# Performance work log

Measured on AMD Instinct MI355X. Metric: run time of the kernel, lower is better.

Reference implementation:

```python
import jax, jax.numpy as jnp
import numpy as np

IN_F = 4096
OUT_F = 4096
NNZ = int(0.01 * IN_F * OUT_F)
ALPHA = 1.0


def setup_inputs() -> dict:
    key = jax.random.key(0)
    k1, k2, k3, k4, k5 = jax.random.split(key, 5)
    x = jax.random.normal(k1, (4, 2048, IN_F), dtype=jnp.float32)
    base_weights = (jax.random.normal(k2, (OUT_F, IN_F), dtype=jnp.float32) * 0.02).astype(jnp.float16)
    # sparse outlier correction in COO form (equivalent content to the CSR buffers)
    ortho_vals = (jax.random.normal(k3, (NNZ,), dtype=jnp.float32) * 1e-3).astype(jnp.float16)
    ortho_rows = jax.random.randint(k4, (NNZ,), 0, OUT_F, dtype=jnp.int32)
    ortho_cols = jax.random.randint(k5, (NNZ,), 0, IN_F, dtype=jnp.int32)
    return {"x": x, "base_weights": base_weights, "ortho_vals": ortho_vals,
            "ortho_rows": ortho_rows, "ortho_cols": ortho_cols}


def reference(x, base_weights, ortho_vals, ortho_rows, ortho_cols):
    orig_shape = x.shape
    orig_dtype = x.dtype
    x_flat = x.reshape(-1, IN_F)  # [N, in]

    # Base stream: fp16 GEMM, then cast to fp32 (matches torch.mm on fp16)
    out_base = jnp.matmul(x_flat.astype(jnp.float16), base_weights.T).astype(jnp.float32)

    # Ortho stream: sparse (out,in) correction applied in fp32.
    # Scatter the sparse values into a dense fp32 matrix once (cheap: 64MB),
    # then use a dense GEMM — same math as torch.sparse.mm(W_csr, x^T)^T.
    w_ortho = jnp.zeros((OUT_F, IN_F), dtype=jnp.float32).at[ortho_rows, ortho_cols].add(
        ortho_vals.astype(jnp.float32))
    out_ortho = jnp.matmul(x_flat.astype(jnp.float32), w_ortho.T)  # [N, out]

    out_flat = out_base + ALPHA * out_ortho
    return out_flat.reshape(orig_shape[:-1] + (OUT_F,)).astype(orig_dtype)
```

## Files before the change

kernel.cpp:

```cpp
#include <hip/hip_runtime.h>

typedef _Float16 f16;
typedef unsigned short u16;
typedef unsigned int u32;
typedef long long i64;
typedef __attribute__((ext_vector_type(8))) _Float16 f16x8;
typedef __attribute__((ext_vector_type(4))) float f32x4;
typedef __attribute__((ext_vector_type(16))) float f32x16;

#define IN_F 4096
#define OUT_F 4096

__device__ __forceinline__ void gload16(const f16* g, f16* l) {
  __builtin_amdgcn_global_load_lds(
      (const __attribute__((address_space(1))) void*)g,
      (__attribute__((address_space(3))) void*)l, 16, 0, 0);
}

__global__ __launch_bounds__(256) void cvt_f32_f16(
    const float* __restrict__ in, f16* __restrict__ out, i64 n8) {
  i64 s = (i64)gridDim.x * blockDim.x;
  for (i64 j = (i64)blockIdx.x * blockDim.x + threadIdx.x; j < n8; j += s) {
    float4 a = ((const float4*)in)[2 * j];
    float4 b = ((const float4*)in)[2 * j + 1];
    f16x8 o;
    o[0] = (f16)a.x; o[1] = (f16)a.y; o[2] = (f16)a.z; o[3] = (f16)a.w;
    o[4] = (f16)b.x; o[5] = (f16)b.y; o[6] = (f16)b.z; o[7] = (f16)b.w;
    ((f16x8*)out)[j] = o;
  }
}

__global__ __launch_bounds__(256) void zero32(u32* __restrict__ p, i64 n) {
  i64 s = (i64)gridDim.x * blockDim.x;
  for (i64 j = (i64)blockIdx.x * blockDim.x + threadIdx.x; j < n; j += s) p[j] = 0u;
}

__global__ __launch_bounds__(256) void scatter_woh(
    const float* __restrict__ vals, const int* __restrict__ rows,
    const int* __restrict__ cols, f16* __restrict__ woh, int nnz) {
  int i = blockIdx.x * blockDim.x + threadIdx.x;
  if (i >= nnz) return;
  int r = rows[i], c = cols[i];
  if (r < 0 || r >= OUT_F || c < 0 || c >= IN_F) return;
  float v = vals[i];
  size_t idx = (size_t)r * IN_F + c;
  u32* p = (u32*)woh + (idx >> 1);
  u32 sh = (u32)(idx & 1) * 16u;
  union { f16 h; u16 u; } cv;
  u32 old = *p;
  while (true) {
    u32 assumed = old;
    cv.u = (u16)((assumed >> sh) & 0xFFFFu);
    float cur = (float)cv.h;
    cv.h = (f16)(cur + v);
    u32 nw = (assumed & ~(0xFFFFu << sh)) | ((u32)cv.u << sh);
    old = atomicCAS(p, assumed, nw);
    if (old == assumed) break;
  }
}

template <int STREAM>
__global__ __launch_bounds__(512, 2) void gemm_256(
    const f16* __restrict__ Xh, const f16* __restrict__ Bm,
    float* __restrict__ out, int M) {
  __shared__ alignas(16) f16 As[2][16384];
  __shared__ alignas(16) f16 Bs[2][16384];

  const int tid = threadIdx.x;
  const int lane = tid & 63;
  const int wave = tid >> 6;
  const int wr = wave >> 2;
  const int wc = wave & 3;
  const int l31 = lane & 31, hi5 = lane >> 5, l7 = lane & 7;

  const int bid = (int)blockIdx.x;
  const int nbn = OUT_F / 256;
  const int nbm = M / 256;
  int browi, bcoli;
  if (nbm == 32 && nbn == 16) {
    const int xcd = bid & 7;
    const int j   = bid >> 3;
    const int jr  = j >> 3, jc = j & 7;
    browi = (xcd & 3) * 8 + jr;
    bcoli = (xcd >> 2) * 8 + jc;
  } else {
    const int nwg = nbm * nbn;
    const int swz = ((nwg & 7) == 0) ? ((bid & 7) * (nwg >> 3) + (bid >> 3)) : bid;
    browi = swz / nbn;
    bcoli = swz % nbn;
  }
  const int brow = browi << 8;
  const int bcol = bcoli << 8;

  int aglob[4], bglob[4], ldst[4];
#pragma unroll
  for (int i = 0; i < 4; ++i) {
    int c = i * 512 + tid;
    int row = c >> 3;
    int kc = (c & 7) ^ (row & 7);
    ldst[i] = c * 8;
    aglob[i] = (brow + row) * IN_F + kc * 8;
    bglob[i] = (bcol + row) * IN_F + kc * 8;
  }

  const int abase = (wr * 128 + l31) * 64;
  const int bbase = (wc * 64 + l31) * 64;
  int slot[4];
#pragma unroll
  for (int ks = 0; ks < 4; ++ks) slot[ks] = ((ks * 2 + hi5) ^ l7) * 8;

  f32x16 acc[4][2] = {};

  gload16(Bm + bglob[0], &Bs[0][ldst[0]]);
  gload16(Bm + bglob[1], &Bs[0][ldst[1]]);
  gload16(Bm + bglob[2], &Bs[0][ldst[2]]);
  gload16(Bm + bglob[3], &Bs[0][ldst[3]]);
  gload16(Xh + aglob[0], &As[0][ldst[0]]);
  gload16(Xh + aglob[2], &As[0][ldst[2]]);
  gload16(Xh + aglob[1], &As[0][ldst[1]]);
  gload16(Xh + aglob[3], &As[0][ldst[3]]);
  asm volatile("s_waitcnt vmcnt(2)" ::: "memory");
  __builtin_amdgcn_sched_barrier(0);
  __builtin_amdgcn_s_barrier();

#define MFMA32(MT)                                                             \
  __builtin_amdgcn_s_setprio(1);                                               \
  _Pragma("unroll")                                                            \
  for (int ks = 0; ks < 4; ++ks)                                               \
    _Pragma("unroll")                                                          \
    for (int nt = 0; nt < 2; ++nt)                                             \
      acc[MT][nt] = __builtin_amdgcn_mfma_f32_32x32x16_f16(                    \
          af[ks], bf[nt][ks], acc[MT][nt], 0, 0, 0);                           \
  __builtin_amdgcn_s_setprio(0);

  const int NT = IN_F / 64;
  for (int kt = 0; kt < NT; ++kt) {
    const f16* A = &As[kt & 1][0];
    const f16* B = &Bs[kt & 1][0];
    f16* An = &As[(kt & 1) ^ 1][0];
    f16* Bn = &Bs[(kt & 1) ^ 1][0];
    const int kn = (kt + 1) * 64;
    const bool pf = (kt + 1 < NT);

    f16x8 bf[2][4];
    f16x8 af[4];

#pragma unroll
    for (int nt = 0; nt < 2; ++nt)
#pragma unroll
      for (int ks = 0; ks < 4; ++ks)
        bf[nt][ks] = *(const f16x8*)(B + bbase + nt * 2048 + slot[ks]);
#pragma unroll
    for (int ks = 0; ks < 4; ++ks)
      af[ks] = *(const f16x8*)(A + abase + 0 * 2048 + slot[ks]);
    if (pf) { gload16(Bm + bglob[0] + kn, Bn + ldst[0]);
              gload16(Bm + bglob[1] + kn, Bn + ldst[1]); }
    __builtin_amdgcn_s_barrier();
    MFMA32(0)
    __builtin_amdgcn_s_barrier();

#pragma unroll
    for (int ks = 0; ks < 4; ++ks)
      af[ks] = *(const f16x8*)(A + abase + 1 * 2048 + slot[ks]);
    if (pf) { gload16(Bm + bglob[2] + kn, Bn + ldst[2]);
              gload16(Bm + bglob[3] + kn, Bn + ldst[3]); }
    if (pf) asm volatile("s_waitcnt vmcnt(4)" ::: "memory");
    else    asm volatile("s_waitcnt vmcnt(0)" ::: "memory");
    __builtin_amdgcn_sched_barrier(0);
    __builtin_amdgcn_s_barrier();
    MFMA32(1)
    __builtin_amdgcn_s_barrier();

#pragma unroll
    for (int ks = 0; ks < 4; ++ks)
      af[ks] = *(const f16x8*)(A + abase + 2 * 2048 + slot[ks]);
    if (pf) { gload16(Xh + aglob[0] + kn, An + ldst[0]);
              gload16(Xh + aglob[2] + kn, An + ldst[2]); }
    __builtin_amdgcn_s_barrier();
    MFMA32(2)
    __builtin_amdgcn_s_barrier();

#pragma unroll
    for (int ks = 0; ks < 4; ++ks)
      af[ks] = *(const f16x8*)(A + abase + 3 * 2048 + slot[ks]);
    if (pf) { gload16(Xh + aglob[1] + kn, An + ldst[1]);
              gload16(Xh + aglob[3] + kn, An + ldst[3]); }
    if (pf) {
      asm volatile("s_waitcnt vmcnt(2)" ::: "memory");
      __builtin_amdgcn_sched_barrier(0);
    }
    __builtin_amdgcn_s_barrier();
    MFMA32(3)
    __builtin_amdgcn_s_barrier();
  }
#undef MFMA32

  const int ccol0 = bcol + wc * 64 + l31;
#pragma unroll
  for (int mt = 0; mt < 4; ++mt)
#pragma unroll
    for (int nt = 0; nt < 2; ++nt)
#pragma unroll
      for (int reg = 0; reg < 16; ++reg) {
        const int row = brow + wr * 128 + mt * 32 + (reg & 3) + 8 * (reg >> 2) + 4 * hi5;
        float* p = out + (size_t)row * OUT_F + (ccol0 + nt * 32);
        if constexpr (STREAM == 0)
          *p = (float)(f16)acc[mt][nt][reg];
        else
          *p += acc[mt][nt][reg];
      }
}

template <bool A16, int STREAM>
__global__ __launch_bounds__(256, 2) void gemm_one(
    const float* __restrict__ Xf, const f16* __restrict__ Xh,
    const f16* __restrict__ Bm, float* __restrict__ out, int M) {
  constexpr int LDA = A16 ? 32 : 40;
  __shared__ alignas(16) f16 As[128 * LDA];
  __shared__ alignas(16) f16 Bs[128 * 32];

  const int tid = threadIdx.x, lane = tid & 63, wave = tid >> 6;
  const int wr = wave >> 1, wc = wave & 1;
  const int nbn = OUT_F / 128;
  const int nwg = (int)gridDim.x;
  const int bid = (int)blockIdx.x;
  const int swz = ((nwg & 7) == 0) ? ((bid & 7) * (nwg >> 3) + (bid >> 3)) : bid;
  const int brow = (swz / nbn) << 7;
  const int bcol = (swz % nbn) << 7;

  f32x4 acc[4][4] = {};
  const int srow = tid >> 2, sk = (tid & 3) * 8;
  const f16* gB = Bm + (size_t)(bcol + srow) * IN_F + sk;
  f16* sB = Bs + tid * 8;
  const f16*   gA = A16 ? (Xh + (size_t)(brow + srow) * IN_F + sk) : (const f16*)nullptr;
  const float* gX = A16 ? (const float*)nullptr : (Xf + (size_t)(brow + srow) * IN_F + sk);
  f16* sA  = As + tid * 8;
  f16* sAr = As + srow * LDA + sk;
  const f16* pa = As + (wr * 64 + (lane & 15)) * LDA + (lane >> 4) * 8;
  const f16* pb = Bs + (wc * 64 + (lane & 15)) * 32 + (lane >> 4) * 8;

  for (int k0 = 0; k0 < IN_F; k0 += 32) {
    if constexpr (A16) {
      gload16(gA + k0, sA);
      gload16(gA + k0 + (size_t)64 * IN_F, sA + 2048);
    } else {
      float4 u0 = *(const float4*)(gX + k0);
      float4 u1 = *(const float4*)(gX + k0 + 4);
      float4 v0 = *(const float4*)(gX + k0 + (size_t)64 * IN_F);
      float4 v1 = *(const float4*)(gX + k0 + (size_t)64 * IN_F + 4);
      f16x8 h0, h1;
      h0[0] = (f16)u0.x; h0[1] = (f16)u0.y; h0[2] = (f16)u0.z; h0[3] = (f16)u0.w;
      h0[4] = (f16)u1.x; h0[5] = (f16)u1.y; h0[6] = (f16)u1.z; h0[7] = (f16)u1.w;
      h1[0] = (f16)v0.x; h1[1] = (f16)v0.y; h1[2] = (f16)v0.z; h1[3] = (f16)v0.w;
      h1[4] = (f16)v1.x; h1[5] = (f16)v1.y; h1[6] = (f16)v1.z; h1[7] = (f16)v1.w;
      *(f16x8*)sAr = h0;
      *(f16x8*)(sAr + 64 * LDA) = h1;
    }
    gload16(gB + k0, sB);
    gload16(gB + k0 + (size_t)64 * IN_F, sB + 2048);
    __syncthreads();
    f16x8 af[4], bfr[4];
#pragma unroll
    for (int m = 0; m < 4; ++m) af[m] = *(const f16x8*)(pa + m * 16 * LDA);
#pragma unroll
    for (int n = 0; n < 4; ++n) bfr[n] = *(const f16x8*)(pb + n * 512);
#pragma unroll
    for (int m = 0; m < 4; ++m)
#pragma unroll
      for (int n = 0; n < 4; ++n)
        acc[m][n] = __builtin_amdgcn_mfma_f32_16x16x32_f16(af[m], bfr[n], acc[m][n], 0, 0, 0);
    __syncthreads();
  }
  const int crow0 = brow + wr * 64 + ((lane >> 4) << 2);
  const int ccol0 = bcol + wc * 64 + (lane & 15);
#pragma unroll
  for (int m = 0; m < 4; ++m)
#pragma unroll
    for (int n = 0; n < 4; ++n)
#pragma unroll
      for (int r = 0; r < 4; ++r) {
        float* p = out + (size_t)(crow0 + m * 16 + r) * OUT_F + (ccol0 + n * 16);
        if constexpr (STREAM == 0) *p = (float)(f16)acc[m][n][r];
        else *p += acc[m][n][r];
      }
}

extern "C" void kernel_launch(void* const* d_in, const int* in_sizes, int n_in,
                              void* d_out, int out_size, void* d_ws, size_t ws_size,
                              hipStream_t stream) {
  const float* x    = (const float*)d_in[0];
  const float* W    = (const float*)d_in[1];
  const float* vals = (const float*)d_in[2];
  const int*   rows = (const int*)d_in[3];
  const int*   cols = (const int*)d_in[4];
  float*       out  = (float*)d_out;

  const i64 total_x = (i64)in_sizes[0];
  const int M   = (int)(total_x / IN_F);
  const int nnz = in_sizes[2];
  if (M <= 0 || M % 128 != 0) return;

  const size_t whb = (size_t)OUT_F * IN_F * 2;
  const size_t xhb = (size_t)M * IN_F * 2;

  if (ws_size >= xhb + 2 * whb) {
    f16* xh  = (f16*)d_ws;
    f16* wh  = (f16*)((char*)d_ws + xhb);
    f16* woh = (f16*)((char*)d_ws + xhb + whb);
    cvt_f32_f16<<<2048, 256, 0, stream>>>(x, xh, total_x / 8);
    cvt_f32_f16<<<2048, 256, 0, stream>>>(W, wh, (i64)OUT_F * IN_F / 8);
    zero32<<<2048, 256, 0, stream>>>((u32*)woh, (i64)(whb / 4));
    scatter_woh<<<(nnz + 255) / 256, 256, 0, stream>>>(vals, rows, cols, woh, nnz);
    if (M % 256 == 0) {
      const int grid = (M / 256) * (OUT_F / 256);
      gemm_256<0><<<grid, 512, 0, stream>>>(xh, wh, out, M);
      gemm_256<1><<<grid, 512, 0, stream>>>(xh, woh, out, M);
    } else {
      const int grid = (M / 128) * (OUT_F / 128);
      gemm_one<true, 0><<<grid, 256, 0, stream>>>(nullptr, xh, wh, out, M);
      gemm_one<true, 1><<<grid, 256, 0, stream>>>(nullptr, xh, woh, out, M);
    }
  } else if (ws_size >= 2 * whb) {
    f16* wh  = (f16*)d_ws;
    f16* woh = (f16*)((char*)d_ws + whb);
    cvt_f32_f16<<<2048, 256, 0, stream>>>(W, wh, (i64)OUT_F * IN_F / 8);
    zero32<<<2048, 256, 0, stream>>>((u32*)woh, (i64)(whb / 4));
    scatter_woh<<<(nnz + 255) / 256, 256, 0, stream>>>(vals, rows, cols, woh, nnz);
    const int grid = (M / 128) * (OUT_F / 128);
    gemm_one<false, 0><<<grid, 256, 0, stream>>>(x, nullptr, wh, out, M);
    gemm_one<false, 1><<<grid, 256, 0, stream>>>(x, nullptr, woh, out, M);
  }
}
```

Baseline: 587.5 us.

## Switch 256-tile GEMM to 16x16x32 MFMA with quadrant-ordered fragment schedule

Result: slower. 600.2 us (+2.2%).

```diff
diff --git a/kernel.cpp b/kernel.cpp
--- a/kernel.cpp
+++ b/kernel.cpp
@@ -6,7 +6,6 @@
 typedef long long i64;
 typedef __attribute__((ext_vector_type(8))) _Float16 f16x8;
 typedef __attribute__((ext_vector_type(4))) float f32x4;
-typedef __attribute__((ext_vector_type(16))) float f32x16;
 
 #define IN_F 4096
 #define OUT_F 4096
@@ -71,7 +70,7 @@
   const int wave = tid >> 6;
   const int wr = wave >> 2;
   const int wc = wave & 3;
-  const int l31 = lane & 31, hi5 = lane >> 5, l7 = lane & 7;
+  const int lo = lane & 15, hi = lane >> 4, l7 = lane & 7;
 
   const int bid = (int)blockIdx.x;
   const int nbn = OUT_F / 256;
@@ -96,41 +95,43 @@
 #pragma unroll
   for (int i = 0; i < 4; ++i) {
     int c = i * 512 + tid;
-    int row = c >> 3;
-    int kc = (c & 7) ^ (row & 7);
+    int u = c >> 3;
+    int kc = (c & 7) ^ (u & 7);
     ldst[i] = c * 8;
-    aglob[i] = (brow + row) * IN_F + kc * 8;
-    bglob[i] = (bcol + row) * IN_F + kc * 8;
-  }
-
-  const int abase = (wr * 128 + l31) * 64;
-  const int bbase = (wc * 64 + l31) * 64;
-  int slot[4];
-#pragma unroll
-  for (int ks = 0; ks < 4; ++ks) slot[ks] = ((ks * 2 + hi5) ^ l7) * 8;
-
-  f32x16 acc[4][2] = {};
-
+    aglob[i] = (brow + u) * IN_F + kc * 8;
+    int rB = (((u >> 5) & 3) << 6) + (((u >> 7) & 1) << 5) + (u & 31);
+    bglob[i] = (bcol + rB) * IN_F + kc * 8;
+  }
+
+  const int abase = (wr * 128 + lo) * 64;
+  const int bbase = (wc * 32 + lo) * 64;
+  const int slot0 = (hi ^ l7) * 8;
+  const int slot1 = ((4 + hi) ^ l7) * 8;
+
+  f32x4 acc[8][4] = {};
+
+  gload16(Xh + aglob[0], &As[0][ldst[0]]);
+  gload16(Xh + aglob[2], &As[0][ldst[2]]);
   gload16(Bm + bglob[0], &Bs[0][ldst[0]]);
   gload16(Bm + bglob[1], &Bs[0][ldst[1]]);
   gload16(Bm + bglob[2], &Bs[0][ldst[2]]);
   gload16(Bm + bglob[3], &Bs[0][ldst[3]]);
-  gload16(Xh + aglob[0], &As[0][ldst[0]]);
-  gload16(Xh + aglob[2], &As[0][ldst[2]]);
   gload16(Xh + aglob[1], &As[0][ldst[1]]);
   gload16(Xh + aglob[3], &As[0][ldst[3]]);
-  asm volatile("s_waitcnt vmcnt(2)" ::: "memory");
+  asm volatile("s_waitcnt vmcnt(4)" ::: "memory");
   __builtin_amdgcn_sched_barrier(0);
   __builtin_amdgcn_s_barrier();
 
-#define MFMA32(MT)                                                             \
+#define CLUSTER(BF, MO, NO)                                                    \
   __builtin_amdgcn_s_setprio(1);                                               \
   _Pragma("unroll")                                                            \
-  for (int ks = 0; ks < 4; ++ks)                                               \
+  for (int ks = 0; ks < 2; ++ks)                                               \
     _Pragma("unroll")                                                          \
-    for (int nt = 0; nt < 2; ++nt)                                             \
-      acc[MT][nt] = __builtin_amdgcn_mfma_f32_32x32x16_f16(                    \
-          af[ks], bf[nt][ks], acc[MT][nt], 0, 0, 0);                           \
+    for (int mf = 0; mf < 4; ++mf)                                             \
+      _Pragma("unroll")                                                        \
+      for (int nf = 0; nf < 2; ++nf)                                           \
+        acc[(MO) + mf][(NO) + nf] = __builtin_amdgcn_mfma_f32_16x16x32_f16(    \
+            af[mf][ks], BF[nf][ks], acc[(MO) + mf][(NO) + nf], 0, 0, 0);       \
   __builtin_amdgcn_s_setprio(0);
 
   const int NT = IN_F / 64;
@@ -142,72 +143,82 @@
     const int kn = (kt + 1) * 64;
     const bool pf = (kt + 1 < NT);
 
-    f16x8 bf[2][4];
-    f16x8 af[4];
-
-#pragma unroll
-    for (int nt = 0; nt < 2; ++nt)
-#pragma unroll
-      for (int ks = 0; ks < 4; ++ks)
-        bf[nt][ks] = *(const f16x8*)(B + bbase + nt * 2048 + slot[ks]);
-#pragma unroll
-    for (int ks = 0; ks < 4; ++ks)
-      af[ks] = *(const f16x8*)(A + abase + 0 * 2048 + slot[ks]);
+    f16x8 af[4][2], bf0[2][2], bf1[2][2];
+
+#pragma unroll
+    for (int mf = 0; mf < 4; ++mf) {
+      af[mf][0] = *(const f16x8*)(A + abase + mf * 1024 + slot0);
+      af[mf][1] = *(const f16x8*)(A + abase + mf * 1024 + slot1);
+    }
+#pragma unroll
+    for (int nf = 0; nf < 2; ++nf) {
+      bf0[nf][0] = *(const f16x8*)(B + bbase + nf * 1024 + slot0);
+      bf0[nf][1] = *(const f16x8*)(B + bbase + nf * 1024 + slot1);
+    }
+    if (pf) { gload16(Xh + aglob[0] + kn, An + ldst[0]);
+              gload16(Xh + aglob[2] + kn, An + ldst[2]); }
+    if (pf) asm volatile("s_waitcnt vmcnt(4)" ::: "memory");
+    else    asm volatile("s_waitcnt vmcnt(2)" ::: "memory");
+    __builtin_amdgcn_sched_barrier(0);
+    __builtin_amdgcn_s_barrier();
+    CLUSTER(bf0, 0, 0)
+    __builtin_amdgcn_s_barrier();
+
+#pragma unroll
+    for (int nf = 0; nf < 2; ++nf) {
+      bf1[nf][0] = *(const f16x8*)(B + bbase + 8192 + nf * 1024 + slot0);
+      bf1[nf][1] = *(const f16x8*)(B + bbase + 8192 + nf * 1024 + slot1);
+    }
     if (pf) { gload16(Bm + bglob[0] + kn, Bn + ldst[0]);
               gload16(Bm + bglob[1] + kn, Bn + ldst[1]); }
-    __builtin_amdgcn_s_barrier();
-    MFMA32(0)
-    __builtin_amdgcn_s_barrier();
-
-#pragma unroll
-    for (int ks = 0; ks < 4; ++ks)
-      af[ks] = *(const f16x8*)(A + abase + 1 * 2048 + slot[ks]);
-    if (pf) { gload16(Bm + bglob[2] + kn, Bn + ldst[2]);
-              gload16(Bm + bglob[3] + kn, Bn + ldst[3]); }
     if (pf) asm volatile("s_waitcnt vmcnt(4)" ::: "memory");
     else    asm volatile("s_waitcnt vmcnt(0)" ::: "memory");
     __builtin_amdgcn_sched_barrier(0);
     __builtin_amdgcn_s_barrier();
-    MFMA32(1)
-    __builtin_amdgcn_s_barrier();
-
-#pragma unroll
-    for (int ks = 0; ks < 4; ++ks)
-      af[ks] = *(const f16x8*)(A + abase + 2 * 2048 + slot[ks]);
-    if (pf) { gload16(Xh + aglob[0] + kn, An + ldst[0]);
-              gload16(Xh + aglob[2] + kn, An + ldst[2]); }
-    __builtin_amdgcn_s_barrier();
-    MFMA32(2)
-    __builtin_amdgcn_s_barrier();
-
-#pragma unroll
-    for (int ks = 0; ks < 4; ++ks)
-      af[ks] = *(const f16x8*)(A + abase + 3 * 2048 + slot[ks]);
+    CLUSTER(bf1, 0, 2)
+    __builtin_amdgcn_s_barrier();
+
+#pragma unroll
+    for (int mf = 0; mf < 4; ++mf) {
+      af[mf][0] = *(const f16x8*)(A + abase + 4096 + mf * 1024 + slot0);
+      af[mf][1] = *(const f16x8*)(A + abase + 4096 + mf * 1024 + slot1);
+    }
+    if (pf) { gload16(Bm + bglob[2] + kn, Bn + ldst[2]);
+              gload16(Bm + bglob[3] + kn, Bn + ldst[3]); }
+    __builtin_amdgcn_s_barrier();
+    CLUSTER(bf1, 4, 2)
+    __builtin_amdgcn_s_barrier();
+
+#pragma unroll
+    for (int nf = 0; nf < 2; ++nf) {
+      bf0[nf][0] = *(const f16x8*)(B + bbase + nf * 1024 + slot0);
+      bf0[nf][1] = *(const f16x8*)(B + bbase + nf * 1024 + slot1);
+    }
     if (pf) { gload16(Xh + aglob[1] + kn, An + ldst[1]);
               gload16(Xh + aglob[3] + kn, An + ldst[3]); }
     if (pf) {
-      asm volatile("s_waitcnt vmcnt(2)" ::: "memory");
+      asm volatile("s_waitcnt vmcnt(4)" ::: "memory");
       __builtin_amdgcn_sched_barrier(0);
     }
     __builtin_amdgcn_s_barrier();
-    MFMA32(3)
-    __builtin_amdgcn_s_barrier();
-  }
-#undef MFMA32
-
-  const int ccol0 = bcol + wc * 64 + l31;
-#pragma unroll
-  for (int mt = 0; mt < 4; ++mt)
-#pragma unroll
-    for (int nt = 0; nt < 2; ++nt)
-#pragma unroll
-      for (int reg = 0; reg < 16; ++reg) {
-        const int row = brow + wr * 128 + mt * 32 + (reg & 3) + 8 * (reg >> 2) + 4 * hi5;
-        float* p = out + (size_t)row * OUT_F + (ccol0 + nt * 32);
+    CLUSTER(bf0, 4, 0)
+    __builtin_amdgcn_s_barrier();
+  }
+#undef CLUSTER
+
+  const int crow0 = brow + wr * 128 + (hi << 2);
+  const int ccol0 = bcol + wc * 64 + lo;
+#pragma unroll
+  for (int mf = 0; mf < 8; ++mf)
+#pragma unroll
+    for (int nf = 0; nf < 4; ++nf)
+#pragma unroll
+      for (int r = 0; r < 4; ++r) {
+        float* p = out + (size_t)(crow0 + mf * 16 + r) * OUT_F + (ccol0 + nf * 16);
         if constexpr (STREAM == 0)
-          *p = (float)(f16)acc[mt][nt][reg];
+          *p = (float)(f16)acc[mf][nf][r];
         else
-          *p += acc[mt][nt][reg];
+          *p += acc[mf][nf][r];
       }
 }
 
```
